# Kernel optimization log

Hardware: AMD Instinct MI355X
Metric: run time of the kernel (lower is better)

The kernel has to match this reference:

```python
import jax, jax.numpy as jnp
import numpy as np

N_NODES = 32768
EMB_DIM = 128
N_CODES = 4096
N_GRAPHS = 512
ALPHA = 0.5            # args.alpha_init buffer
COMMIT_W = 1.0         # args.commitment_weight
BN_EPS = 1e-5


def setup_inputs() -> dict:
    key = jax.random.key(0)
    ks = jax.random.split(key, 8)
    node_feat = jax.random.normal(ks[0], (N_NODES, EMB_DIM), dtype=jnp.float32)
    score = jax.random.uniform(ks[1], (N_NODES, 1), dtype=jnp.float32)
    batch = jnp.sort(jax.random.randint(ks[2], (N_NODES,), 0, N_GRAPHS)).astype(jnp.int64)
    codebook_c = jax.random.normal(ks[3], (N_CODES, EMB_DIM), dtype=jnp.float32)
    codebook_s = jax.random.normal(ks[4], (N_CODES, EMB_DIM), dtype=jnp.float32)
    w1 = jax.random.normal(ks[5], (EMB_DIM, 2 * EMB_DIM), dtype=jnp.float32) * (1.0 / np.sqrt(EMB_DIM))
    b1 = jnp.zeros((2 * EMB_DIM,), dtype=jnp.float32)
    gamma = jnp.ones((2 * EMB_DIM,), dtype=jnp.float32)
    beta = jnp.zeros((2 * EMB_DIM,), dtype=jnp.float32)
    run_mean = jnp.zeros((2 * EMB_DIM,), dtype=jnp.float32)
    run_var = jnp.ones((2 * EMB_DIM,), dtype=jnp.float32)
    w2 = jax.random.normal(ks[6], (2 * EMB_DIM, 1), dtype=jnp.float32) * (1.0 / np.sqrt(2 * EMB_DIM))
    b2 = jnp.zeros((1,), dtype=jnp.float32)
    return {"node_feat": node_feat, "score": score, "batch": batch,
            "codebook_c": codebook_c, "codebook_s": codebook_s,
            "w1": w1, "b1": b1, "gamma": gamma, "beta": beta,
            "run_mean": run_mean, "run_var": run_var, "w2": w2, "b2": b2}


def _vector_quantize(x, codebook):
    # squared euclidean distance [N, K]; argmin lookup with straight-through.
    d2 = (jnp.sum(x * x, axis=-1, keepdims=True)
          - 2.0 * (x @ codebook.T)
          + jnp.sum(codebook * codebook, axis=-1))
    idx = jnp.argmin(d2, axis=-1)                     # [N]
    quantize = codebook[idx]                          # gather [N, D]
    commit_loss = jnp.mean((jax.lax.stop_gradient(quantize) - x) ** 2) * COMMIT_W
    out = x + jax.lax.stop_gradient(quantize - x)     # straight-through estimator
    return out, idx, commit_loss


def _mean_pool(x, batch):
    sums = jax.ops.segment_sum(x, batch, num_segments=N_GRAPHS)
    counts = jax.ops.segment_sum(jnp.ones((x.shape[0], 1), x.dtype), batch, num_segments=N_GRAPHS)
    return sums / jnp.maximum(counts, 1.0)


def reference(node_feat, score, batch, codebook_c, codebook_s,
              w1, b1, gamma, beta, run_mean, run_var, w2, b2):
    h_c = node_feat * score + ALPHA * node_feat * (1.0 - score)
    h_s = node_feat * (1.0 - score) + ALPHA * node_feat * score
    vq_c, _, cmt_loss_c = _vector_quantize(h_c, codebook_c)
    vq_s, _, cmt_loss_s = _vector_quantize(h_s, codebook_s)
    c_node_feat = node_feat * score + vq_c
    s_node_feat = node_feat * (1.0 - score) + vq_s
    c_graph_feat = _mean_pool(c_node_feat, batch)
    s_graph_feat = _mean_pool(s_node_feat, batch)
    # classifier: Linear -> BatchNorm1d (eval) -> ReLU -> Dropout(identity) -> Linear
    h = c_graph_feat @ w1 + b1
    h = (h - run_mean) * jax.lax.rsqrt(run_var + BN_EPS) * gamma + beta
    h = jax.nn.relu(h)
    c_logit = h @ w2 + b2
    return (c_logit, c_graph_feat, s_graph_feat, cmt_loss_c, cmt_loss_s, c_node_feat, s_node_feat)
```

## Files before the change

### kernel.cpp

```cpp
#include <hip/hip_runtime.h>
#include <hip/hip_bf16.h>

#define NODES   32768
#define DIM     128
#define NCODES  4096
#define NGRAPHS 512
#define THR     0.0625f

#define OFF_LOGIT 0
#define OFF_CG    512
#define OFF_SG    66048
#define OFF_LC    131584
#define OFF_LS    131585
#define OFF_CN    131586
#define OFF_SN    4325890

#define SPLIT_U16   263680
#define PLANE_U16   524288
#define HALF_F32    1180416
#define CSLOT_F32   1442560

#define WS_CNORM    0
#define WS_IDX      32768
#define WS_FLAGCNT  294928
#define WS_STARTS   294936
#define WS_FLAGLIST 296988
#define FLAG_CAP    32767

typedef __attribute__((ext_vector_type(8))) _Float16 f16x8_t;
typedef __attribute__((ext_vector_type(4))) float f32x4_t;

__device__ __forceinline__ float h_of(float x, float sc, int cb) {
    float omsc = __fsub_rn(1.0f, sc);
    float half_x = __fmul_rn(0.5f, x);
    if (cb == 0)
        return __fadd_rn(__fmul_rn(x, sc), __fmul_rn(half_x, omsc));
    else
        return __fadd_rn(__fmul_rn(x, omsc), __fmul_rn(half_x, sc));
}

__device__ __forceinline__ unsigned short f2h(float f) {
    return __builtin_bit_cast(unsigned short, (_Float16)f);
}

__device__ __forceinline__ void gload_lds16(const void* g, void* l) {
    __builtin_amdgcn_global_load_lds(
        (const __attribute__((address_space(1))) int*)g,
        (__attribute__((address_space(3))) int*)l, 16, 0, 0);
}

__device__ __forceinline__ unsigned sortkey(float f) {
    unsigned b = __float_as_uint(f);
    return (b & 0x80000000u) ? ~b : (b | 0x80000000u);
}
__device__ __forceinline__ float keyinv(unsigned k) {
    unsigned b = (k & 0x80000000u) ? (k & 0x7FFFFFFFu) : ~k;
    return __uint_as_float(b);
}

__global__ __launch_bounds__(256) void prep_kernel(
    const float* __restrict__ cb_c, const float* __restrict__ cb_s,
    const int* __restrict__ batch,
    float* __restrict__ cnorm, unsigned short* __restrict__ splits,
    int* __restrict__ starts, int* __restrict__ flagcnt)
{
    int gwave = (blockIdx.x * 256 + threadIdx.x) >> 6;
    int lane  = threadIdx.x & 63;

    if (gwave < 2 * NCODES) {
        int cb = gwave >> 12, row = gwave & (NCODES - 1);
        const float* cp = (cb ? cb_s : cb_c) + (size_t)row * DIM;
        float2 v = ((const float2*)cp)[lane];
        float p = __fadd_rn(__fmul_rn(v.x, v.x), __fmul_rn(v.y, v.y));
        #pragma unroll
        for (int off = 32; off; off >>= 1) p = __fadd_rn(p, __shfl_xor(p, off, 64));
        if (lane == 0) cnorm[cb * NCODES + row] = p;
        unsigned int* hp = (unsigned int*)(splits + (size_t)cb * PLANE_U16);
        hp[row * 64 + lane] = (unsigned)f2h(v.x) | ((unsigned)f2h(v.y) << 16);
    } else {
        int w1 = gwave - 2 * NCODES;
        int g = w1 * 64 + lane;
        if (g <= NGRAPHS) {
            int lo = 0, hi = NODES;
            while (lo < hi) { int mid = (lo + hi) >> 1; if (batch[mid] < g) lo = mid + 1; else hi = mid; }
            starts[g] = lo;
        }
        if (w1 == 0 && lane < 2) flagcnt[lane] = 0;
    }
}

__global__ __launch_bounds__(256, 4) void vq_main_kernel(
    const float* __restrict__ node_feat, const float* __restrict__ score,
    const unsigned short* __restrict__ splits, const float* __restrict__ cnorm,
    unsigned long long* __restrict__ halfres)
{
    __shared__ unsigned short lds[16384];
    const int nb    = blockIdx.x & 255;
    const int half  = blockIdx.x >> 8;
    const int cb    = blockIdx.y;
    const int nbase = nb * 128;
    const int tid = threadIdx.x;
    const int w   = tid >> 6;
    const int l15 = tid & 15;
    const int lg  = (tid & 63) >> 4;
    const int swz = (tid & 7) << 4;
    const float* cnp = cnorm + cb * NCODES + half * 2048;

    #pragma unroll
    for (int i = 0; i < 16; ++i) {
        int idx = i * 1024 + tid * 4;
        int row = idx >> 7, k = idx & 127;
        float4 x = *(const float4*)&node_feat[(size_t)(nbase + row) * DIM + k];
        float sc = score[nbase + row];
        unsigned u0 = f2h(h_of(x.x, sc, cb)), u1 = f2h(h_of(x.y, sc, cb));
        unsigned u2 = f2h(h_of(x.z, sc, cb)), u3 = f2h(h_of(x.w, sc, cb));
        int abyte = row * 256 + ((2 * k) ^ ((row & 7) << 4));
        uint2 hw; hw.x = u0 | (u1 << 16); hw.y = u2 | (u3 << 16);
        *(uint2*)((char*)lds + abyte) = hw;
    }
    __syncthreads();

    f16x8_t ahi[2][4];
    int colbyte[4];
    #pragma unroll
    for (int ch = 0; ch < 4; ++ch) colbyte[ch] = (ch * 64 + lg * 16) ^ swz;
    #pragma unroll
    for (int rs = 0; rs < 2; ++rs)
        #pragma unroll
        for (int ch = 0; ch < 4; ++ch) {
            int row = 32 * w + 16 * rs + l15;
            ahi[rs][ch] = *(const f16x8_t*)((const char*)lds + row * 256 + colbyte[ch]);
        }
    __syncthreads();

    const unsigned short* wplane = splits + (size_t)cb * PLANE_U16 + half * 262144;
    int soff[4];
    #pragma unroll
    for (int i = 0; i < 4; ++i) {
        int row = w * 16 + i * 4 + lg;
        soff[i] = row * 256 + ((l15 * 16) ^ ((row & 7) << 4));
    }

    {
        const char* tb = (const char*)wplane;
        #pragma unroll
        for (int i = 0; i < 4; ++i)
            gload_lds16(tb + soff[i], (char*)lds + w * 4096 + i * 1024);
    }
    __syncthreads();

    const float NEG_INF = -3.4e38f;
    float b1v[2][4], b2v[2][4]; int b1i[2][4];
    #pragma unroll
    for (int rs = 0; rs < 2; ++rs)
        #pragma unroll
        for (int r = 0; r < 4; ++r) { b1v[rs][r] = NEG_INF; b2v[rs][r] = NEG_INF; b1i[rs][r] = 0; }

    for (int t = 0; t < 32; ++t) {
        int bs_cur = (t & 1) << 14;
        float cnc[4];
        #pragma unroll
        for (int cs = 0; cs < 4; ++cs) cnc[cs] = __fmul_rn(-0.5f, cnp[t * 64 + cs * 16 + l15]);
        if (t < 31) {
            int bs_nxt = ((t + 1) & 1) << 14;
            const char* tb = (const char*)wplane + (t + 1) * 16384;
            #pragma unroll
            for (int i = 0; i < 4; ++i)
                gload_lds16(tb + soff[i], (char*)lds + bs_nxt + w * 4096 + i * 1024);
        }

        #pragma unroll
        for (int cp = 0; cp < 2; ++cp) {
            f32x4_t acc[2][2];
            #pragma unroll
            for (int rs = 0; rs < 2; ++rs)
                #pragma unroll
                for (int c2 = 0; c2 < 2; ++c2) {
                    float iv = cnc[cp * 2 + c2];
                    acc[rs][c2] = (f32x4_t){iv, iv, iv, iv};
                }

            #pragma unroll
            for (int ch = 0; ch < 4; ++ch)
                #pragma unroll
                for (int c2 = 0; c2 < 2; ++c2) {
                    int cs = cp * 2 + c2;
                    f16x8_t bh = *(const f16x8_t*)((const char*)lds + bs_cur +
                                                   (cs * 16 + l15) * 256 + colbyte[ch]);
                    acc[0][c2] = __builtin_amdgcn_mfma_f32_16x16x32_f16(ahi[0][ch], bh, acc[0][c2], 0, 0, 0);
                    acc[1][c2] = __builtin_amdgcn_mfma_f32_16x16x32_f16(ahi[1][ch], bh, acc[1][c2], 0, 0, 0);
                }

            #pragma unroll
            for (int c2 = 0; c2 < 2; ++c2) {
                int cs = cp * 2 + c2;
                int code = half * 2048 + t * 64 + cs * 16 + l15;
                #pragma unroll
                for (int rs = 0; rs < 2; ++rs)
                    #pragma unroll
                    for (int r = 0; r < 4; ++r) {
                        float a = acc[rs][c2][r];
                        bool gt = a > b1v[rs][r];
                        float nb2 = __builtin_amdgcn_fmed3f(a, b1v[rs][r], b2v[rs][r]);
                        if (gt) b1i[rs][r] = code;
                        b1v[rs][r] = fmaxf(a, b1v[rs][r]);
                        b2v[rs][r] = nb2;
                    }
            }
        }
        __syncthreads();
    }

    #pragma unroll
    for (int off = 1; off < 16; off <<= 1) {
        #pragma unroll
        for (int rs = 0; rs < 2; ++rs)
            #pragma unroll
            for (int r = 0; r < 4; ++r) {
                float ov1 = __shfl_xor(b1v[rs][r], off, 64);
                int   oi  = __shfl_xor(b1i[rs][r], off, 64);
                float ov2 = __shfl_xor(b2v[rs][r], off, 64);
                bool take = (ov1 > b1v[rs][r]) || (ov1 == b1v[rs][r] && oi < b1i[rs][r]);
                float loser = fminf(ov1, b1v[rs][r]);
                b1v[rs][r] = fmaxf(ov1, b1v[rs][r]);
                if (take) b1i[rs][r] = oi;
                b2v[rs][r] = fmaxf(loser, fmaxf(ov2, b2v[rs][r]));
            }
    }
    if (l15 == 0) {
        #pragma unroll
        for (int rs = 0; rs < 2; ++rs)
            #pragma unroll
            for (int r = 0; r < 4; ++r) {
                int node = nbase + 32 * w + 16 * rs + 4 * lg + r;
                unsigned key = sortkey(b1v[rs][r]);
                unsigned pay = (unsigned)b1i[rs][r] |
                               ((b1v[rs][r] - b2v[rs][r] < THR) ? 0x1000u : 0u);
                halfres[((size_t)(cb * 2 + half)) * NODES + node] =
                    ((unsigned long long)key << 32) | pay;
            }
    }
}

__global__ __launch_bounds__(256) void resolve_kernel(
    const unsigned long long* __restrict__ hr, unsigned long long* __restrict__ cslot,
    int* __restrict__ idx_ws, int* __restrict__ flagcnt, int* __restrict__ flaglist)
{
    int cb = blockIdx.y;
    int node = blockIdx.x * 256 + threadIdx.x;
    unsigned long long A = hr[((size_t)(cb * 2 + 0)) * NODES + node];
    unsigned long long B = hr[((size_t)(cb * 2 + 1)) * NODES + node];
    unsigned ka = (unsigned)(A >> 32), kb = (unsigned)(B >> 32);
    bool awin = ka >= kb;
    unsigned long long W = awin ? A : B;
    float aw = keyinv(awin ? ka : kb);
    float al = keyinv(awin ? kb : ka);
    bool flag = ((W >> 12) & 1ull) || (__fsub_rn(aw, al) < THR);
    idx_ws[cb * NODES + node] = (int)(W & 0xFFFu);
    if (flag) cslot[(size_t)cb * NODES + node] = ~0ull;

    unsigned long long mask = __ballot(flag);
    if (mask) {
        int lane = threadIdx.x & 63;
        int leader = __ffsll((long long)mask) - 1;
        int base = 0;
        if (lane == leader) base = atomicAdd(flagcnt + cb, (int)__popcll(mask));
        base = __shfl(base, leader, 64);
        if (flag) {
            int pos = base + (int)__popcll(mask & ((1ull << lane) - 1ull));
            if (pos < FLAG_CAP) flaglist[cb * FLAG_CAP + pos] = node;
        }
    }
}

__global__ __launch_bounds__(256) void vq_cleanup_kernel(
    const float* __restrict__ node_feat, const float* __restrict__ score,
    const float* __restrict__ cb_c, const float* __restrict__ cb_s,
    const float* __restrict__ cnorm, const int* __restrict__ flagcnt,
    const int* __restrict__ flaglist, unsigned long long* __restrict__ slots)
{
    __shared__ char cbS[32768];
    __shared__ float hbuf[8][128];
    const int cb  = blockIdx.y;
    const int seg = blockIdx.x & 63;
    const int ng  = blockIdx.x >> 6;
    const float* cbp = cb ? cb_s : cb_c;
    const int* list = flaglist + cb * FLAG_CAP;
    int cnt = flagcnt[cb]; if (cnt > FLAG_CAP) cnt = FLAG_CAP;
    const int tid = threadIdx.x, w = tid >> 6, l = tid & 63;

    {
        int c = tid >> 2, ks = (tid & 3) * 32;
        const float* src = cbp + (size_t)(seg * 64 + c) * DIM + ks;
        char* dst = cbS + c * 512;
        int sw = (c & 7) << 4;
        #pragma unroll
        for (int j = 0; j < 8; ++j) {
            float4 v = *(const float4*)(src + j * 4);
            *(float4*)(dst + ((ks * 4 + j * 16) ^ sw)) = v;
        }
    }
    const int mycode = seg * 64 + l;
    const float cn = cnorm[cb * NCODES + mycode];
    const int swl = (l & 7) << 4;
    const char* crow = cbS + l * 512;
    __syncthreads();

    for (int base = ng * 8; base < cnt; base += 128) {
        int eA = base + 2 * w, eB = eA + 1;
        bool vA = eA < cnt, vB = eB < cnt;
        int nA = list[vA ? eA : 0], nB = list[vB ? eB : 0];
        float scA = score[nA], scB = score[nB];
        float a0 = h_of(node_feat[(size_t)nA * DIM + l],      scA, cb);
        float a1 = h_of(node_feat[(size_t)nA * DIM + 64 + l], scA, cb);
        float b0 = h_of(node_feat[(size_t)nB * DIM + l],      scB, cb);
        float b1 = h_of(node_feat[(size_t)nB * DIM + 64 + l], scB, cb);
        hbuf[2 * w][l] = a0;     hbuf[2 * w][64 + l] = a1;
        hbuf[2 * w + 1][l] = b0; hbuf[2 * w + 1][64 + l] = b1;
        float sxA = __fadd_rn(__fmul_rn(a0, a0), __fmul_rn(a1, a1));
        float sxB = __fadd_rn(__fmul_rn(b0, b0), __fmul_rn(b1, b1));
        #pragma unroll
        for (int off = 32; off; off >>= 1) {
            sxA = __fadd_rn(sxA, __shfl_xor(sxA, off, 64));
            sxB = __fadd_rn(sxB, __shfl_xor(sxB, off, 64));
        }
        asm volatile("s_waitcnt lgkmcnt(0)" ::: "memory");

        float pA0 = 0.f, pA1 = 0.f, pA2 = 0.f, pA3 = 0.f;
        float pB0 = 0.f, pB1 = 0.f, pB2 = 0.f, pB3 = 0.f;
        const float4* hA = (const float4*)hbuf[2 * w];
        const float4* hB = (const float4*)hbuf[2 * w + 1];
        #pragma unroll 8
        for (int m = 0; m < 32; ++m) {
            float4 c4 = *(const float4*)(crow + ((m * 16) ^ swl));
            float4 ha = hA[m], hb = hB[m];
            pA0 = fmaf(ha.x, c4.x, pA0); pA1 = fmaf(ha.y, c4.y, pA1);
            pA2 = fmaf(ha.z, c4.z, pA2); pA3 = fmaf(ha.w, c4.w, pA3);
            pB0 = fmaf(hb.x, c4.x, pB0); pB1 = fmaf(hb.y, c4.y, pB1);
            pB2 = fmaf(hb.z, c4.z, pB2); pB3 = fmaf(hb.w, c4.w, pB3);
        }
        float dotA = __fadd_rn(__fadd_rn(pA0, pA1), __fadd_rn(pA2, pA3));
        float dotB = __fadd_rn(__fadd_rn(pB0, pB1), __fadd_rn(pB2, pB3));
        float dA = __fadd_rn(__fsub_rn(sxA, __fmul_rn(2.0f, dotA)), cn);
        float dB = __fadd_rn(__fsub_rn(sxB, __fmul_rn(2.0f, dotB)), cn);

        unsigned long long pkA = ((unsigned long long)sortkey(dA) << 32) | (unsigned)mycode;
        unsigned long long pkB = ((unsigned long long)sortkey(dB) << 32) | (unsigned)mycode;
        #pragma unroll
        for (int off = 1; off < 64; off <<= 1) {
            unsigned long long oA = __shfl_xor(pkA, off, 64);
            unsigned long long oB = __shfl_xor(pkB, off, 64);
            pkA = (oA < pkA) ? oA : pkA;
            pkB = (oB < pkB) ? oB : pkB;
        }
        if (l == 0 && vA) atomicMin(&slots[(size_t)cb * NODES + nA], pkA);
        if (l == 0 && vB) atomicMin(&slots[(size_t)cb * NODES + nB], pkB);
        asm volatile("s_waitcnt lgkmcnt(0)" ::: "memory");
    }
}

__global__ __launch_bounds__(256) void flag_writeback_kernel(
    const int* __restrict__ flagcnt, const int* __restrict__ flaglist,
    const unsigned long long* __restrict__ slots, int* __restrict__ idx_ws)
{
    int gt = blockIdx.x * 256 + threadIdx.x;
    int c0 = flagcnt[0]; if (c0 > FLAG_CAP) c0 = FLAG_CAP;
    int c1 = flagcnt[1]; if (c1 > FLAG_CAP) c1 = FLAG_CAP;
    for (int e = gt; e < 2 * FLAG_CAP; e += 256 * 256) {
        int cb = (e >= FLAG_CAP) ? 1 : 0;
        int i = e - cb * FLAG_CAP;
        int cnt = cb ? c1 : c0;
        if (i < cnt) {
            int node = flaglist[cb * FLAG_CAP + i];
            idx_ws[cb * NODES + node] =
                (int)(slots[(size_t)cb * NODES + node] & 0xFFFFFFFFull);
        }
    }
}

__global__ __launch_bounds__(256) void gather_kernel(
    const float* __restrict__ node_feat, const float* __restrict__ score,
    const float* __restrict__ cb_c, const float* __restrict__ cb_s,
    const int* __restrict__ idx_all, float* __restrict__ out,
    double* __restrict__ partials)
{
    __shared__ float redc[4], reds[4];
    int wave = threadIdx.x >> 6, lane = threadIdx.x & 63;
    int node = blockIdx.x * 4 + wave;
    float sc = score[node];
    float2 x  = *(const float2*)&node_feat[(size_t)node * DIM + 2 * lane];
    int ic = idx_all[node], is_ = idx_all[NODES + node];
    float2 qc = *(const float2*)&cb_c[(size_t)ic * DIM + 2 * lane];
    float2 qs = *(const float2*)&cb_s[(size_t)is_ * DIM + 2 * lane];

    float omsc = __fsub_rn(1.0f, sc);
    float2 cn, sn;
    cn.x = __fadd_rn(__fmul_rn(x.x, sc), qc.x);
    cn.y = __fadd_rn(__fmul_rn(x.y, sc), qc.y);
    sn.x = __fadd_rn(__fmul_rn(x.x, omsc), qs.x);
    sn.y = __fadd_rn(__fmul_rn(x.y, omsc), qs.y);
    *(float2*)&out[OFF_CN + (size_t)node * DIM + 2 * lane] = cn;
    *(float2*)&out[OFF_SN + (size_t)node * DIM + 2 * lane] = sn;

    float hc1 = h_of(x.x, sc, 0), hc2 = h_of(x.y, sc, 0);
    float hs1 = h_of(x.x, sc, 1), hs2 = h_of(x.y, sc, 1);
    float d1 = qc.x - hc1, d2 = qc.y - hc2;
    float e1 = qs.x - hs1, e2 = qs.y - hs2;
    float lc = d1 * d1 + d2 * d2;
    float ls = e1 * e1 + e2 * e2;
    #pragma unroll
    for (int off = 32; off; off >>= 1) {
        lc += __shfl_down(lc, off, 64);
        ls += __shfl_down(ls, off, 64);
    }
    if (lane == 0) { redc[wave] = lc; reds[wave] = ls; }
    __syncthreads();
    if (threadIdx.x == 0) {
        partials[blockIdx.x]        = (double)redc[0] + redc[1] + redc[2] + redc[3];
        partials[8192 + blockIdx.x] = (double)reds[0] + reds[1] + reds[2] + reds[3];
    }
}

__global__ __launch_bounds__(256) void loss_reduce_kernel(
    const double* __restrict__ partials, float* __restrict__ out)
{
    __shared__ double red[4];
    int b = blockIdx.x, t = threadIdx.x, w = t >> 6, l = t & 63;
    const double* p = partials + b * 8192;
    double s = 0.0;
    #pragma unroll 4
    for (int i = t; i < 8192; i += 256) s += p[i];
    #pragma unroll
    for (int off = 32; off; off >>= 1) s += __shfl_down(s, off, 64);
    if (l == 0) red[w] = s;
    __syncthreads();
    if (t == 0) {
        double tot = (red[0] + red[1]) + (red[2] + red[3]);
        out[OFF_LC + b] = (float)(tot * (1.0 / 4194304.0));
    }
}

__global__ __launch_bounds__(256) void pool_kernel(
    const int* __restrict__ starts, float* __restrict__ out)
{
    int g = blockIdx.x;
    int half = threadIdx.x >> 7, d = threadIdx.x & 127;
    int s = starts[g], e = starts[g + 1];
    const float* src = out + (half ? OFF_SN : OFF_CN);
    float sum = 0.0f;
    for (int n = s; n < e; ++n) sum = __fadd_rn(sum, src[(size_t)n * DIM + d]);
    float cnt = fmaxf((float)(e - s), 1.0f);
    out[(half ? OFF_SG : OFF_CG) + g * DIM + d] = __fdiv_rn(sum, cnt);
}

__global__ __launch_bounds__(256) void classifier_kernel(
    const float* __restrict__ w1, const float* __restrict__ b1,
    const float* __restrict__ gamma, const float* __restrict__ beta,
    const float* __restrict__ rm, const float* __restrict__ rv,
    const float* __restrict__ w2, const float* __restrict__ b2,
    float* __restrict__ out)
{
    __shared__ float row[DIM];
    __shared__ float red[4];
    int g = blockIdx.x, t = threadIdx.x;
    if (t < DIM) row[t] = out[OFF_CG + g * DIM + t];
    __syncthreads();
    float h = 0.0f;
    #pragma unroll 8
    for (int k = 0; k < DIM; ++k) h = fmaf(row[k], w1[k * 256 + t], h);
    h = __fadd_rn(h, b1[t]);
    float inv = __frsqrt_rn(__fadd_rn(rv[t], 1e-5f));
    h = __fadd_rn(__fmul_rn(__fmul_rn(__fsub_rn(h, rm[t]), inv), gamma[t]), beta[t]);
    h = fmaxf(h, 0.0f);
    float p = __fmul_rn(h, w2[t]);
    #pragma unroll
    for (int off = 32; off; off >>= 1) p += __shfl_down(p, off, 64);
    if ((t & 63) == 0) red[t >> 6] = p;
    __syncthreads();
    if (t == 0) {
        float total = __fadd_rn(__fadd_rn(red[0], red[1]), __fadd_rn(red[2], red[3]));
        out[OFF_LOGIT + g] = __fadd_rn(total, b2[0]);
    }
}

extern "C" void kernel_launch(void* const* d_in, const int* in_sizes, int n_in,
                              void* d_out, int out_size, void* d_ws, size_t ws_size,
                              hipStream_t stream) {
    const float* node_feat = (const float*)d_in[0];
    const float* score     = (const float*)d_in[1];
    const int*   batch     = (const int*)d_in[2];
    const float* cb_c      = (const float*)d_in[3];
    const float* cb_s      = (const float*)d_in[4];
    const float* w1        = (const float*)d_in[5];
    const float* b1        = (const float*)d_in[6];
    const float* gamma     = (const float*)d_in[7];
    const float* beta      = (const float*)d_in[8];
    const float* rm        = (const float*)d_in[9];
    const float* rv        = (const float*)d_in[10];
    const float* w2        = (const float*)d_in[11];
    const float* b2        = (const float*)d_in[12];
    float* out = (float*)d_out;
    char*  ws  = (char*)d_ws;

    float*  cnorm    = (float*)(ws + WS_CNORM);
    int*    idx      = (int*)(ws + WS_IDX);
    int*    flagcnt  = (int*)(ws + WS_FLAGCNT);
    int*    starts   = (int*)(ws + WS_STARTS);
    int*    flaglist = (int*)(ws + WS_FLAGLIST);
    unsigned short* splits = (unsigned short*)d_out + SPLIT_U16;
    unsigned long long* halfres = (unsigned long long*)(out + HALF_F32);
    unsigned long long* cslot   = (unsigned long long*)(out + CSLOT_F32);
    double* partials = (double*)(out + OFF_CG);

    prep_kernel<<<2051, 256, 0, stream>>>(cb_c, cb_s, batch, cnorm, splits,
                                          starts, flagcnt);
    vq_main_kernel<<<dim3(512, 2), 256, 0, stream>>>(node_feat, score, splits, cnorm,
                                                     halfres);
    resolve_kernel<<<dim3(128, 2), 256, 0, stream>>>(halfres, cslot, idx,
                                                     flagcnt, flaglist);
    vq_cleanup_kernel<<<dim3(1024, 2), 256, 0, stream>>>(node_feat, score, cb_c, cb_s,
                                                         cnorm, flagcnt, flaglist, cslot);
    flag_writeback_kernel<<<256, 256, 0, stream>>>(flagcnt, flaglist, cslot, idx);
    gather_kernel<<<8192, 256, 0, stream>>>(node_feat, score, cb_c, cb_s, idx, out, partials);
    loss_reduce_kernel<<<2, 256, 0, stream>>>(partials, out);
    pool_kernel<<<512, 256, 0, stream>>>(starts, out);
    classifier_kernel<<<512, 256, 0, stream>>>(w1, b1, gamma, beta, rm, rv, w2, b2, out);
}
```

Baseline: 338.7 us.

## Double node tile in VQ main kernel, widen cleanup grid, parallelize pooling

The VQ distance kernel now processes 256 nodes per block (64 rows per wave) instead of 128, so each codebook tile staged in LDS is reused across twice as many MFMAs. This comes at the cost of more registers, a 64KB LDS footprint and half as many blocks. The cleanup kernel grid is widened fourfold with a matching stride change, to spread flagged-node work across more blocks. Mean pooling now splits each graph's nodes across four thread groups, one block per graph and half, and combines the partial sums in LDS, which shortens the serial summation chain per thread.

```diff
diff --git a/kernel.cpp b/kernel.cpp
--- a/kernel.cpp
+++ b/kernel.cpp
@@ -89,16 +89,16 @@
     }
 }
 
-__global__ __launch_bounds__(256, 4) void vq_main_kernel(
+__global__ __launch_bounds__(256, 2) void vq_main_kernel(
     const float* __restrict__ node_feat, const float* __restrict__ score,
     const unsigned short* __restrict__ splits, const float* __restrict__ cnorm,
     unsigned long long* __restrict__ halfres)
 {
-    __shared__ unsigned short lds[16384];
-    const int nb    = blockIdx.x & 255;
-    const int half  = blockIdx.x >> 8;
+    __shared__ __align__(16) char lds[65536];
+    const int nb    = blockIdx.x & 127;
+    const int half  = blockIdx.x >> 7;
     const int cb    = blockIdx.y;
-    const int nbase = nb * 128;
+    const int nbase = nb * 256;
     const int tid = threadIdx.x;
     const int w   = tid >> 6;
     const int l15 = tid & 15;
@@ -107,7 +107,7 @@
     const float* cnp = cnorm + cb * NCODES + half * 2048;
 
     #pragma unroll
-    for (int i = 0; i < 16; ++i) {
+    for (int i = 0; i < 32; ++i) {
         int idx = i * 1024 + tid * 4;
         int row = idx >> 7, k = idx & 127;
         float4 x = *(const float4*)&node_feat[(size_t)(nbase + row) * DIM + k];
@@ -116,20 +116,20 @@
         unsigned u2 = f2h(h_of(x.z, sc, cb)), u3 = f2h(h_of(x.w, sc, cb));
         int abyte = row * 256 + ((2 * k) ^ ((row & 7) << 4));
         uint2 hw; hw.x = u0 | (u1 << 16); hw.y = u2 | (u3 << 16);
-        *(uint2*)((char*)lds + abyte) = hw;
-    }
-    __syncthreads();
-
-    f16x8_t ahi[2][4];
+        *(uint2*)(lds + abyte) = hw;
+    }
+    __syncthreads();
+
+    f16x8_t ahi[4][4];
     int colbyte[4];
     #pragma unroll
     for (int ch = 0; ch < 4; ++ch) colbyte[ch] = (ch * 64 + lg * 16) ^ swz;
     #pragma unroll
-    for (int rs = 0; rs < 2; ++rs)
+    for (int rs = 0; rs < 4; ++rs)
         #pragma unroll
         for (int ch = 0; ch < 4; ++ch) {
-            int row = 32 * w + 16 * rs + l15;
-            ahi[rs][ch] = *(const f16x8_t*)((const char*)lds + row * 256 + colbyte[ch]);
+            int row = 64 * w + 16 * rs + l15;
+            ahi[rs][ch] = *(const f16x8_t*)(lds + row * 256 + colbyte[ch]);
         }
     __syncthreads();
 
@@ -145,14 +145,14 @@
         const char* tb = (const char*)wplane;
         #pragma unroll
         for (int i = 0; i < 4; ++i)
-            gload_lds16(tb + soff[i], (char*)lds + w * 4096 + i * 1024);
+            gload_lds16(tb + soff[i], lds + w * 4096 + i * 1024);
     }
     __syncthreads();
 
     const float NEG_INF = -3.4e38f;
-    float b1v[2][4], b2v[2][4]; int b1i[2][4];
-    #pragma unroll
-    for (int rs = 0; rs < 2; ++rs)
+    float b1v[4][4], b2v[4][4]; int b1i[4][4];
+    #pragma unroll
+    for (int rs = 0; rs < 4; ++rs)
         #pragma unroll
         for (int r = 0; r < 4; ++r) { b1v[rs][r] = NEG_INF; b2v[rs][r] = NEG_INF; b1i[rs][r] = 0; }
 
@@ -166,14 +166,14 @@
             const char* tb = (const char*)wplane + (t + 1) * 16384;
             #pragma unroll
             for (int i = 0; i < 4; ++i)
-                gload_lds16(tb + soff[i], (char*)lds + bs_nxt + w * 4096 + i * 1024);
+                gload_lds16(tb + soff[i], lds + bs_nxt + w * 4096 + i * 1024);
         }
 
         #pragma unroll
         for (int cp = 0; cp < 2; ++cp) {
-            f32x4_t acc[2][2];
+            f32x4_t acc[4][2];
             #pragma unroll
-            for (int rs = 0; rs < 2; ++rs)
+            for (int rs = 0; rs < 4; ++rs)
                 #pragma unroll
                 for (int c2 = 0; c2 < 2; ++c2) {
                     float iv = cnc[cp * 2 + c2];
@@ -185,10 +185,11 @@
                 #pragma unroll
                 for (int c2 = 0; c2 < 2; ++c2) {
                     int cs = cp * 2 + c2;
-                    f16x8_t bh = *(const f16x8_t*)((const char*)lds + bs_cur +
+                    f16x8_t bh = *(const f16x8_t*)(lds + bs_cur +
                                                    (cs * 16 + l15) * 256 + colbyte[ch]);
-                    acc[0][c2] = __builtin_amdgcn_mfma_f32_16x16x32_f16(ahi[0][ch], bh, acc[0][c2], 0, 0, 0);
-                    acc[1][c2] = __builtin_amdgcn_mfma_f32_16x16x32_f16(ahi[1][ch], bh, acc[1][c2], 0, 0, 0);
+                    #pragma unroll
+                    for (int rs = 0; rs < 4; ++rs)
+                        acc[rs][c2] = __builtin_amdgcn_mfma_f32_16x16x32_f16(ahi[rs][ch], bh, acc[rs][c2], 0, 0, 0);
                 }
 
             #pragma unroll
@@ -196,7 +197,7 @@
                 int cs = cp * 2 + c2;
                 int code = half * 2048 + t * 64 + cs * 16 + l15;
                 #pragma unroll
-                for (int rs = 0; rs < 2; ++rs)
+                for (int rs = 0; rs < 4; ++rs)
                     #pragma unroll
                     for (int r = 0; r < 4; ++r) {
                         float a = acc[rs][c2][r];
@@ -214,7 +215,7 @@
     #pragma unroll
     for (int off = 1; off < 16; off <<= 1) {
         #pragma unroll
-        for (int rs = 0; rs < 2; ++rs)
+        for (int rs = 0; rs < 4; ++rs)
             #pragma unroll
             for (int r = 0; r < 4; ++r) {
                 float ov1 = __shfl_xor(b1v[rs][r], off, 64);
@@ -229,10 +230,10 @@
     }
     if (l15 == 0) {
         #pragma unroll
-        for (int rs = 0; rs < 2; ++rs)
+        for (int rs = 0; rs < 4; ++rs)
             #pragma unroll
             for (int r = 0; r < 4; ++r) {
-                int node = nbase + 32 * w + 16 * rs + 4 * lg + r;
+                int node = nbase + 64 * w + 16 * rs + 4 * lg + r;
                 unsigned key = sortkey(b1v[rs][r]);
                 unsigned pay = (unsigned)b1i[rs][r] |
                                ((b1v[rs][r] - b2v[rs][r] < THR) ? 0x1000u : 0u);
@@ -306,7 +307,7 @@
     const char* crow = cbS + l * 512;
     __syncthreads();
 
-    for (int base = ng * 8; base < cnt; base += 128) {
+    for (int base = ng * 8; base < cnt; base += 512) {
         int eA = base + 2 * w, eB = eA + 1;
         bool vA = eA < cnt, vB = eB < cnt;
         int nA = list[vA ? eA : 0], nB = list[vB ? eB : 0];
@@ -440,17 +441,24 @@
     }
 }
 
-__global__ __launch_bounds__(256) void pool_kernel(
+__global__ __launch_bounds__(512) void pool_kernel(
     const int* __restrict__ starts, float* __restrict__ out)
 {
-    int g = blockIdx.x;
-    int half = threadIdx.x >> 7, d = threadIdx.x & 127;
+    __shared__ float part[4][128];
+    int g = blockIdx.x, half = blockIdx.y;
+    int d = threadIdx.x & 127, nl = threadIdx.x >> 7;
     int s = starts[g], e = starts[g + 1];
     const float* src = out + (half ? OFF_SN : OFF_CN);
     float sum = 0.0f;
-    for (int n = s; n < e; ++n) sum = __fadd_rn(sum, src[(size_t)n * DIM + d]);
-    float cnt = fmaxf((float)(e - s), 1.0f);
-    out[(half ? OFF_SG : OFF_CG) + g * DIM + d] = __fdiv_rn(sum, cnt);
+    for (int n = s + nl; n < e; n += 4) sum = __fadd_rn(sum, src[(size_t)n * DIM + d]);
+    part[nl][d] = sum;
+    __syncthreads();
+    if (nl == 0) {
+        float tot = __fadd_rn(__fadd_rn(part[0][d], part[1][d]),
+                              __fadd_rn(part[2][d], part[3][d]));
+        float cnt = fmaxf((float)(e - s), 1.0f);
+        out[(half ? OFF_SG : OFF_CG) + g * DIM + d] = __fdiv_rn(tot, cnt);
+    }
 }
 
 __global__ __launch_bounds__(256) void classifier_kernel(
@@ -514,15 +522,15 @@
 
     prep_kernel<<<2051, 256, 0, stream>>>(cb_c, cb_s, batch, cnorm, splits,
                                           starts, flagcnt);
-    vq_main_kernel<<<dim3(512, 2), 256, 0, stream>>>(node_feat, score, splits, cnorm,
+    vq_main_kernel<<<dim3(256, 2), 256, 0, stream>>>(node_feat, score, splits, cnorm,
                                                      halfres);
     resolve_kernel<<<dim3(128, 2), 256, 0, stream>>>(halfres, cslot, idx,
                                                      flagcnt, flaglist);
-    vq_cleanup_kernel<<<dim3(1024, 2), 256, 0, stream>>>(node_feat, score, cb_c, cb_s,
+    vq_cleanup_kernel<<<dim3(4096, 2), 256, 0, stream>>>(node_feat, score, cb_c, cb_s,
                                                          cnorm, flagcnt, flaglist, cslot);
     flag_writeback_kernel<<<256, 256, 0, stream>>>(flagcnt, flaglist, cslot, idx);
     gather_kernel<<<8192, 256, 0, stream>>>(node_feat, score, cb_c, cb_s, idx, out, partials);
     loss_reduce_kernel<<<2, 256, 0, stream>>>(partials, out);
-    pool_kernel<<<512, 256, 0, stream>>>(starts, out);
+    pool_kernel<<<dim3(512, 2), 512, 0, stream>>>(starts, out);
     classifier_kernel<<<512, 256, 0, stream>>>(w1, b1, gamma, beta, rm, rv, w2, b2, out);
 }
```

Result: faster. 323.8 us (-4.4%).
